# Optimization experiments

Hardware: AMD Instinct MI355X
Metric: run time of the kernel (lower is better)

The kernel has to match this reference:

```python
import jax, jax.numpy as jnp
import numpy as np
from jax import lax

B, T, F, H, O = 64, 2048, 128, 128, 128


def setup_inputs() -> dict:
    key = jax.random.key(0)
    ks = jax.random.split(key, 14)
    s = 1.0 / np.sqrt(H)  # torch default GRU/Linear init scale
    u = lambda k_, shp: jax.random.uniform(k_, shp, jnp.float32, -s, s)
    # sorted descending, as required by pack_padded_sequence(enforce_sorted=True)
    lengths = jnp.sort(jax.random.randint(ks[1], (B,), T // 2, T + 1))[::-1]
    return {
        'to_x': jax.random.normal(ks[0], (B, T, F), jnp.float32),
        'lengths': lengths,
        'enc_Wih': u(ks[2], (3 * H, F)), 'enc_Whh': u(ks[3], (3 * H, H)),
        'enc_bih': u(ks[4], (3 * H,)), 'enc_bhh': u(ks[5], (3 * H,)),
        'fc_W': u(ks[6], (H, H)), 'fc_b': u(ks[7], (H,)),
        'dec_Wih': u(ks[8], (3 * H, H)), 'dec_Whh': u(ks[9], (3 * H, H)),
        'dec_bih': u(ks[10], (3 * H,)), 'dec_bhh': u(ks[11], (3 * H,)),
        'out_W': u(ks[12], (O, H)), 'out_b': u(ks[13], (O,)),
    }


def _gru_gates(gi, gh, h):
    # PyTorch GRU cell: r,z gates then candidate n; gate order in weights is [r|z|n]
    ir, iz, inn = jnp.split(gi, 3, -1)
    hr, hz, hn = jnp.split(gh, 3, -1)
    r = jax.nn.sigmoid(ir + hr)
    z = jax.nn.sigmoid(iz + hz)
    n = jnp.tanh(inn + r * hn)
    return (1.0 - z) * n + z * h


def _forward(to_x, lengths, enc_Wih, enc_Whh, enc_bih, enc_bhh, fc_W, fc_b,
             dec_Wih, dec_Whh, dec_bih, dec_bhh, out_W, out_b):
    Bv, Tv, _ = to_x.shape
    Hv = enc_Whh.shape[1]
    # precompute all input projections for the encoder in one big GEMM
    gi_all = jnp.einsum('btf,gf->tbg', to_x, enc_Wih) + enc_bih  # [T,B,3H]
    valid = jnp.arange(Tv)[:, None] < lengths[None, :]  # [T,B]; packed-seq mask

    def enc_step(h, inp):
        gi_t, v_t = inp
        gh = h @ enc_Whh.T + enc_bhh
        h_new = _gru_gates(gi_t, gh, h)
        # packed GRU: hidden frozen once t >= length (final hidden per sequence)
        return jnp.where(v_t[:, None], h_new, h), None

    h_enc, _ = lax.scan(enc_step, jnp.zeros((Bv, Hv), to_x.dtype), (gi_all, valid))

    encoded = h_enc @ fc_W.T + fc_b  # encodeFc on last-layer final hidden

    def dec_cell(x, h):
        gi = x @ dec_Wih.T + dec_bih
        gh = h @ dec_Whh.T + dec_bhh
        return _gru_gates(gi, gh, h)

    # first decoder step: input = encoded, initial hidden = encoder final hidden
    y0 = dec_cell(encoded, h_enc)

    # previous output as both input and (implicitly) hidden state
    def dec_step(h, _):
        h_new = dec_cell(h, h)
        return h_new, h_new

    _, ys = lax.scan(dec_step, y0, None, length=Tv - 1)  # [T-1,B,H]
    dec_out = jnp.concatenate([y0[None], ys], axis=0)  # [T,B,H]
    return jnp.einsum('tbh,oh->bto', dec_out, out_W) + out_b  # [B,T,O]


def reference(to_x, lengths, enc_Wih, enc_Whh, enc_bih, enc_bhh, fc_W, fc_b,
              dec_Wih, dec_Whh, dec_bih, dec_bhh, out_W, out_b):
    return _forward(to_x, lengths, enc_Wih, enc_Whh, enc_bih, enc_bhh, fc_W, fc_b,
                    dec_Wih, dec_Whh, dec_bih, dec_bhh, out_W, out_b)
```

## Files before the change

### kernel.cpp

```cpp
#include <hip/hip_runtime.h>

namespace {

constexpr int kT = 2048;
constexpr int kH = 128;
constexpr int kB = 64;
constexpr int kG = 384;

__device__ __forceinline__ float fsigmoid(float x) {
    return 1.0f / (1.0f + __expf(-x));
}

__device__ __forceinline__ float ftanh(float x) {
    float xc = fminf(fmaxf(x, -15.0f), 15.0f);
    float e = __expf(2.0f * xc);
    return (e - 1.0f) / (e + 1.0f);
}

__device__ __forceinline__ void lds_barrier() {
    __builtin_amdgcn_sched_barrier(0);
    asm volatile("s_waitcnt lgkmcnt(0)" ::: "memory");
    __builtin_amdgcn_s_barrier();
    __builtin_amdgcn_sched_barrier(0);
}

__device__ __forceinline__ float qred(float x) {
    int y1 = __builtin_amdgcn_update_dpp(0, __float_as_int(x), 0xB1, 0xF, 0xF, true);
    x += __int_as_float(y1);
    int y2 = __builtin_amdgcn_update_dpp(0, __float_as_int(x), 0x4E, 0xF, 0xF, true);
    return x + __int_as_float(y2);
}

#define FMA4(acc, wrow, base)                      \
    acc = fmaf(v.x, wrow[(base) + 0], acc);        \
    acc = fmaf(v.y, wrow[(base) + 1], acc);        \
    acc = fmaf(v.z, wrow[(base) + 2], acc);        \
    acc = fmaf(v.w, wrow[(base) + 3], acc);

#define ST4(arr, base, vv)        \
    arr[(base) + 0] = (vv).x;     \
    arr[(base) + 1] = (vv).y;     \
    arr[(base) + 2] = (vv).z;     \
    arr[(base) + 3] = (vv).w;

#define ST4ADD(arr, base, va, vb)          \
    arr[(base) + 0] = (va).x + (vb).x;     \
    arr[(base) + 1] = (va).y + (vb).y;     \
    arr[(base) + 2] = (va).z + (vb).z;     \
    arr[(base) + 3] = (va).w + (vb).w;

__global__ __launch_bounds__(256, 2) void gi_gemm(
    const float* __restrict__ A, const float* __restrict__ W,
    const float* __restrict__ bias, float* __restrict__ G,
    int t0, int steps)
{
    __shared__ float As[128][68];
    __shared__ float Ws[128][68];
    const int m0 = blockIdx.x * 64;
    const int n0 = blockIdx.y * 64;
    const int b  = m0 / steps;
    const int tl = m0 % steps;
    const int tid = threadIdx.x;
    const float* Arow0 = A + ((size_t)b * kT + t0 + tl) * kH;

#pragma unroll
    for (int jj = 0; jj < 8; ++jj) {
        const int i = tid + jj * 256;
        const int r = i >> 5, cb = (i & 31) * 4;
        const float4 va = *reinterpret_cast<const float4*>(Arow0 + (size_t)r * kH + cb);
        As[cb + 0][r] = va.x; As[cb + 1][r] = va.y; As[cb + 2][r] = va.z; As[cb + 3][r] = va.w;
        const float4 vw = *reinterpret_cast<const float4*>(W + (size_t)(n0 + r) * kH + cb);
        Ws[cb + 0][r] = vw.x; Ws[cb + 1][r] = vw.y; Ws[cb + 2][r] = vw.z; Ws[cb + 3][r] = vw.w;
    }
    __syncthreads();

    const int tx = tid & 15, ty = tid >> 4;
    float acc[4][4] = {};
#pragma unroll 2
    for (int k = 0; k < 128; ++k) {
        const float4 a  = *reinterpret_cast<const float4*>(&As[k][ty * 4]);
        const float4 bv = *reinterpret_cast<const float4*>(&Ws[k][tx * 4]);
        const float av[4] = {a.x, a.y, a.z, a.w};
        const float bb[4] = {bv.x, bv.y, bv.z, bv.w};
#pragma unroll
        for (int r = 0; r < 4; ++r)
#pragma unroll
            for (int c = 0; c < 4; ++c) acc[r][c] = fmaf(av[r], bb[c], acc[r][c]);
    }
    const float4 b4 = *reinterpret_cast<const float4*>(bias + n0 + tx * 4);
    const float badd[4] = {b4.x, b4.y, b4.z, b4.w};
#pragma unroll
    for (int r = 0; r < 4; ++r) {
        float4 o;
        o.x = acc[r][0] + badd[0]; o.y = acc[r][1] + badd[1];
        o.z = acc[r][2] + badd[2]; o.w = acc[r][3] + badd[3];
        *reinterpret_cast<float4*>(G + (size_t)(m0 + ty * 4 + r) * kG + n0 + tx * 4) = o;
    }
}

__global__ __attribute__((amdgpu_flat_work_group_size(512, 512), amdgpu_waves_per_eu(2, 2)))
void enc_slab_kernel(
    const float* __restrict__ gslab, const int* __restrict__ lengths,
    const float* __restrict__ Whh, const float* __restrict__ bhh,
    float* __restrict__ hstate, float* __restrict__ out,
    int t0, int t1, int init, int final_slab)
{
    __shared__ __align__(16) float hb[2][kH];

    const int b = blockIdx.x;
    const int tid = threadIdx.x;
    const int j = tid >> 2;
    const int sub = tid & 3;
    const int kbase = sub * 32;
    const int len = lengths[b];

    float w[3][32];
#pragma unroll
    for (int cc = 0; cc < 8; ++cc) {
        const int kk = kbase + (((cc + 2 * sub) & 7) << 2);
        float4 v;
        v = *reinterpret_cast<const float4*>(Whh + (size_t)j * kH + kk);            ST4(w[0], cc * 4, v);
        v = *reinterpret_cast<const float4*>(Whh + (size_t)(kH + j) * kH + kk);     ST4(w[1], cc * 4, v);
        v = *reinterpret_cast<const float4*>(Whh + (size_t)(2 * kH + j) * kH + kk); ST4(w[2], cc * 4, v);
    }
    const float bh0 = bhh[j];
    const float bh1 = bhh[kH + j];
    const float bh2 = bhh[2 * kH + j];

    const float* gb = gslab + (size_t)b * (t1 - t0) * kG;
    float gr[4], gz[4], gn[4];
#define LOADG(s, tt)                                              \
    do {                                                          \
        const int tc = ((tt) < t1) ? (tt) : (t1 - 1);             \
        const float* gp = gb + (size_t)(tc - t0) * kG;            \
        gr[s] = gp[j]; gz[s] = gp[kH + j]; gn[s] = gp[2 * kH + j];\
    } while (0)
    LOADG(0, t0); LOADG(1, t0 + 1); LOADG(2, t0 + 2); LOADG(3, t0 + 3);

    if (tid < kH) hb[0][tid] = init ? 0.0f : hstate[(size_t)b * kH + tid];
    __syncthreads();

    int cur = 0;
    int tcap = (len + 3) & ~3;
    if (tcap > t1) tcap = t1;

#define ENC_STEP(s)                                                         \
    do {                                                                    \
        const int t = tb + (s);                                             \
        const float* hcur = hb[cur];                                        \
        float A0 = 0.f, A1 = 0.f, A2 = 0.f;                                 \
        _Pragma("unroll")                                                   \
        for (int cc = 0; cc < 8; ++cc) {                                    \
            const float4 v = *reinterpret_cast<const float4*>(              \
                hcur + kbase + (((cc + 2 * sub) & 7) << 2));                \
            FMA4(A0, w[0], cc * 4);                                         \
            FMA4(A1, w[1], cc * 4);                                         \
            FMA4(A2, w[2], cc * 4);                                         \
        }                                                                   \
        A0 = qred(A0); A1 = qred(A1); A2 = qred(A2);                        \
        const float hq = hcur[j];                                           \
        const float r = fsigmoid(gr[s] + A0 + bh0);                         \
        const float z = fsigmoid(gz[s] + A1 + bh1);                         \
        const float n = ftanh(gn[s] + r * (A2 + bh2));                      \
        const float hnew = (1.0f - z) * n + z * hq;                         \
        const float hc = (t < len) ? hnew : hq;                             \
        LOADG(s, t + 4);                                                    \
        const int nxt = cur ^ 1;                                            \
        if (sub == 0) hb[nxt][j] = hc;                                      \
        lds_barrier();                                                      \
        cur = nxt;                                                          \
    } while (0)

    for (int tb = t0; tb < tcap; tb += 4) {
        ENC_STEP(0); ENC_STEP(1); ENC_STEP(2); ENC_STEP(3);
    }
#undef ENC_STEP
#undef LOADG

    if (tid < kH) {
        hstate[(size_t)b * kH + tid] = hb[cur][tid];
        if (final_slab) out[((size_t)b * kT + 1) * kH + tid] = hb[cur][tid];
    }
}

__global__ __launch_bounds__(512, 2) void enc_fb_kernel(
    const float* __restrict__ to_x, const int* __restrict__ lengths,
    const float* __restrict__ Wih, const float* __restrict__ Whh,
    const float* __restrict__ bih, const float* __restrict__ bhh,
    float* __restrict__ out)
{
    __shared__ __align__(16) float hb2[2][132];
    __shared__ __align__(16) float xr[4][132];

    const int b = blockIdx.x;
    const int tid = threadIdx.x;
    const int j = tid >> 2;
    const int s4 = tid & 3;
    const int xh = s4 >> 1;
    const int sub = s4 & 1;
    const int len = lengths[b];
    const bool loader = (tid >= 480);
    const float* xrow = to_x + (size_t)b * kT * kH + (tid - 480) * 4;

    const float* W  = xh ? Whh : Wih;
    const float* bp = xh ? bhh : bih;

    float w[3][64];
#pragma unroll
    for (int r = 0; r < 3; ++r) {
        const float* rowp = W + (size_t)(r * kH + j) * kH + sub * 64;
#pragma unroll
        for (int k = 0; k < 64; k += 4) {
            const float4 v = *reinterpret_cast<const float4*>(rowp + k);
            ST4(w[r], k, v);
        }
    }
    const float bias0 = bp[j];
    const float bias1 = bp[kH + j];
    const float bias2 = bp[2 * kH + j];

    float4 xf0, xf1, xf2, xf3;
    if (tid < kH) hb2[0][tid] = 0.0f;
    if (loader) {
        xf0 = *reinterpret_cast<const float4*>(xrow + 0 * (size_t)kH);
        xf1 = *reinterpret_cast<const float4*>(xrow + 1 * (size_t)kH);
        xf2 = *reinterpret_cast<const float4*>(xrow + 2 * (size_t)kH);
        xf3 = *reinterpret_cast<const float4*>(xrow + 3 * (size_t)kH);
        *reinterpret_cast<float4*>(&xr[0][(tid - 480) * 4]) = xf0;
    }
    __syncthreads();

    int cur = 0;
    const int lenUp = (len + 3) & ~3;

#define FB_STEP(s, XFCUR, XFNEXT)                                          \
    do {                                                                   \
        const int t = t0 + (s);                                            \
        const float* src = (xh ? &hb2[cur][0] : &xr[s][0]) + sub * 64;     \
        float a0 = 0.f, a1 = 0.f, a2 = 0.f;                                \
        _Pragma("unroll")                                                  \
        for (int c = 0; c < 16; ++c) {                                     \
            const float4 v = *reinterpret_cast<const float4*>(src + c * 4);\
            FMA4(a0, w[0], c * 4);                                         \
            FMA4(a1, w[1], c * 4);                                         \
            FMA4(a2, w[2], c * 4);                                         \
        }                                                                  \
        a0 += __shfl_xor(a0, 1);                                           \
        a1 += __shfl_xor(a1, 1);                                           \
        a2 += __shfl_xor(a2, 1);                                           \
        a0 += bias0; a1 += bias1; a2 += bias2;                             \
        const float b0 = __shfl_xor(a0, 2);                                \
        const float b1 = __shfl_xor(a1, 2);                                \
        const float b2 = __shfl_xor(a2, 2);                                \
        const float hq  = hb2[cur][j];                                     \
        const float r   = fsigmoid(a0 + b0);                               \
        const float z   = fsigmoid(a1 + b1);                               \
        const float inn = xh ? b2 : a2;                                    \
        const float hn  = xh ? a2 : b2;                                    \
        const float n   = ftanh(inn + r * hn);                             \
        const float hnew = (1.0f - z) * n + z * hq;                        \
        const float hc = (t < len) ? hnew : hq;                            \
        if (loader) {                                                      \
            const int tc = ((t + 4) < len) ? (t + 4) : (len - 1);          \
            XFCUR = *reinterpret_cast<const float4*>(xrow + (size_t)tc * kH); \
        }                                                                  \
        const int nxt = cur ^ 1;                                           \
        if (s4 == 0) hb2[nxt][j] = hc;                                     \
        if (loader) *reinterpret_cast<float4*>(&xr[((s) + 1) & 3][(tid - 480) * 4]) = XFNEXT; \
        lds_barrier();                                                     \
        cur = nxt;                                                         \
    } while (0)

    for (int t0 = 0; t0 < lenUp; t0 += 4) {
        FB_STEP(0, xf0, xf1);
        FB_STEP(1, xf1, xf2);
        FB_STEP(2, xf2, xf3);
        FB_STEP(3, xf3, xf0);
    }
#undef FB_STEP

    if (tid < kH) out[((size_t)b * kT + 1) * kH + tid] = hb2[cur][tid];
}

__global__ void y0_kernel(
    const float* __restrict__ fcW, const float* __restrict__ fcb,
    const float* __restrict__ Wih, const float* __restrict__ Whh,
    const float* __restrict__ bih, const float* __restrict__ bhh,
    float* __restrict__ out)
{
    __shared__ float h[kH];
    __shared__ float enc[kH];
    __shared__ float gbuf[768];

    const int b = blockIdx.x;
    const int tid = threadIdx.x;

    if (tid < kH) h[tid] = out[((size_t)b * kT + 1) * kH + tid];
    __syncthreads();

    if (tid < kH) {
        float s = fcb[tid];
        const float* row = fcW + (size_t)tid * kH;
#pragma unroll 4
        for (int k = 0; k < kH; k += 4) {
            const float4 v = *reinterpret_cast<const float4*>(row + k);
            s = fmaf(v.x, h[k + 0], s);
            s = fmaf(v.y, h[k + 1], s);
            s = fmaf(v.z, h[k + 2], s);
            s = fmaf(v.w, h[k + 3], s);
        }
        enc[tid] = s;
    }
    __syncthreads();

    for (int rr = 0; rr < 3; ++rr) {
        const int row = tid + 256 * rr;
        const float* Wr;
        const float* src;
        float s;
        if (row < 384) { Wr = Wih + (size_t)row * kH;         src = enc; s = bih[row]; }
        else           { Wr = Whh + (size_t)(row - 384) * kH; src = h;   s = bhh[row - 384]; }
#pragma unroll 4
        for (int k = 0; k < kH; k += 4) {
            const float4 v = *reinterpret_cast<const float4*>(Wr + k);
            s = fmaf(v.x, src[k + 0], s);
            s = fmaf(v.y, src[k + 1], s);
            s = fmaf(v.z, src[k + 2], s);
            s = fmaf(v.w, src[k + 3], s);
        }
        gbuf[row] = s;
    }
    __syncthreads();

    if (tid < kH) {
        const float r = fsigmoid(gbuf[tid] + gbuf[384 + tid]);
        const float z = fsigmoid(gbuf[128 + tid] + gbuf[512 + tid]);
        const float n = ftanh(gbuf[256 + tid] + r * gbuf[640 + tid]);
        out[(size_t)b * kT * kH + tid] = (1.0f - z) * n + z * h[tid];
    }
}

__global__ __attribute__((amdgpu_flat_work_group_size(512, 512), amdgpu_waves_per_eu(2, 2)))
void dec_kernel(
    const float* __restrict__ Wih, const float* __restrict__ Whh,
    const float* __restrict__ bih, const float* __restrict__ bhh,
    float* __restrict__ out)
{
    __shared__ __align__(16) float hb[2][kH];
    __shared__ int lastbad;

    const int b     = blockIdx.x;
    const int tid   = threadIdx.x;
    const int q     = tid >> 2;
    const int sub   = tid & 3;
    const int kbase = sub * 32;
    constexpr float kTol = 2e-6f;

    float w[4][32];
#pragma unroll
    for (int cc = 0; cc < 8; ++cc) {
        const int kk = kbase + (((cc + 2 * sub) & 7) << 2);
        float4 vi, vh;
        vi = *reinterpret_cast<const float4*>(Wih + (size_t)q * kH + kk);
        vh = *reinterpret_cast<const float4*>(Whh + (size_t)q * kH + kk);
        ST4ADD(w[0], cc * 4, vi, vh);
        vi = *reinterpret_cast<const float4*>(Wih + (size_t)(kH + q) * kH + kk);
        vh = *reinterpret_cast<const float4*>(Whh + (size_t)(kH + q) * kH + kk);
        ST4ADD(w[1], cc * 4, vi, vh);
        vi = *reinterpret_cast<const float4*>(Wih + (size_t)(2 * kH + q) * kH + kk);
        ST4(w[2], cc * 4, vi);
        vh = *reinterpret_cast<const float4*>(Whh + (size_t)(2 * kH + q) * kH + kk);
        ST4(w[3], cc * 4, vh);
    }
    const float brz0 = bih[q] + bhh[q];
    const float brz1 = bih[kH + q] + bhh[kH + q];
    const float bin  = bih[2 * kH + q];
    const float bhn  = bhh[2 * kH + q];

    if (tid < kH) hb[0][tid] = out[(size_t)b * kT * kH + tid];
    if (tid == 0) lastbad = 0;
    __syncthreads();

    float* orow = out + (size_t)b * kT * kH + q;

    int cur = 0;
    int tfill = kT;
    for (int t = 1; t < kT; ++t) {
        const float* hcur = hb[cur];
        float a0 = 0.f, a1 = 0.f, a2 = 0.f, a3 = 0.f;
#pragma unroll
        for (int cc = 0; cc < 8; ++cc) {
            const float4 v = *reinterpret_cast<const float4*>(
                hcur + kbase + (((cc + 2 * sub) & 7) << 2));
            FMA4(a0, w[0], cc * 4);
            FMA4(a1, w[1], cc * 4);
            FMA4(a2, w[2], cc * 4);
            FMA4(a3, w[3], cc * 4);
        }
        a0 = qred(a0); a1 = qred(a1); a2 = qred(a2); a3 = qred(a3);

        const float hq = hcur[q];
        const float r = fsigmoid(a0 + brz0);
        const float z = fsigmoid(a1 + brz1);
        const float n = ftanh(a2 + bin + r * (a3 + bhn));
        const float hnew = (1.0f - z) * n + z * hq;

        const int nxt = cur ^ 1;
        if (sub == 0) {
            hb[nxt][q] = hnew;
            orow[(size_t)t * kH] = hnew;
            if (fabsf(hnew - hq) > kTol) lastbad = t;
        }
        lds_barrier();
        cur = nxt;
        if (lastbad != t) { tfill = t + 1; break; }
    }

    if (tfill < kT) {
        const int c = tid & 31;
        const float4 hv = *reinterpret_cast<const float4*>(&hb[cur][c * 4]);
        for (int tt = tfill + (tid >> 5); tt < kT; tt += 16) {
            *reinterpret_cast<float4*>(out + ((size_t)b * kT + tt) * kH + c * 4) = hv;
        }
    }
}

__global__ __launch_bounds__(256, 1) void proj_kernel(
    const float* __restrict__ Wo, const float* __restrict__ ob,
    float* __restrict__ out)
{
    __shared__ float As[128][68];
    __shared__ float Ws[128][132];
    const int m0 = blockIdx.x * 64;
    const int tid = threadIdx.x;

#pragma unroll
    for (int jj = 0; jj < 8; ++jj) {
        const int i = tid + jj * 256;
        const int r = i >> 5, cb = (i & 31) * 4;
        const float4 v = *reinterpret_cast<const float4*>(out + (size_t)(m0 + r) * kH + cb);
        As[cb + 0][r] = v.x; As[cb + 1][r] = v.y; As[cb + 2][r] = v.z; As[cb + 3][r] = v.w;
    }
#pragma unroll
    for (int jj = 0; jj < 16; ++jj) {
        const int i = tid + jj * 256;
        const int o = i >> 5, cb = (i & 31) * 4;
        const float4 v = *reinterpret_cast<const float4*>(Wo + (size_t)o * kH + cb);
        Ws[cb + 0][o] = v.x; Ws[cb + 1][o] = v.y; Ws[cb + 2][o] = v.z; Ws[cb + 3][o] = v.w;
    }
    __syncthreads();

    const int tx = tid & 15, ty = tid >> 4;
    float acc[4][8] = {};
#pragma unroll 2
    for (int k = 0; k < 128; ++k) {
        const float4 a  = *reinterpret_cast<const float4*>(&As[k][ty * 4]);
        const float4 b0 = *reinterpret_cast<const float4*>(&Ws[k][tx * 4]);
        const float4 b1 = *reinterpret_cast<const float4*>(&Ws[k][64 + tx * 4]);
        const float av[4] = {a.x, a.y, a.z, a.w};
        const float bb[8] = {b0.x, b0.y, b0.z, b0.w, b1.x, b1.y, b1.z, b1.w};
#pragma unroll
        for (int r = 0; r < 4; ++r)
#pragma unroll
            for (int c = 0; c < 8; ++c) acc[r][c] = fmaf(av[r], bb[c], acc[r][c]);
    }
    const float4 o0 = *reinterpret_cast<const float4*>(ob + tx * 4);
    const float4 o1 = *reinterpret_cast<const float4*>(ob + 64 + tx * 4);
    const float ba[8] = {o0.x, o0.y, o0.z, o0.w, o1.x, o1.y, o1.z, o1.w};
#pragma unroll
    for (int r = 0; r < 4; ++r) {
        float4 s0, s1;
        s0.x = acc[r][0] + ba[0]; s0.y = acc[r][1] + ba[1];
        s0.z = acc[r][2] + ba[2]; s0.w = acc[r][3] + ba[3];
        s1.x = acc[r][4] + ba[4]; s1.y = acc[r][5] + ba[5];
        s1.z = acc[r][6] + ba[6]; s1.w = acc[r][7] + ba[7];
        float* rowp = out + (size_t)(m0 + ty * 4 + r) * kH;
        *reinterpret_cast<float4*>(rowp + tx * 4)      = s0;
        *reinterpret_cast<float4*>(rowp + 64 + tx * 4) = s1;
    }
}

}

extern "C" void kernel_launch(void* const* d_in, const int* in_sizes, int n_in,
                              void* d_out, int out_size, void* d_ws, size_t ws_size,
                              hipStream_t stream) {
    (void)in_sizes; (void)n_in; (void)out_size;

    const float* to_x    = (const float*)d_in[0];
    const int*   lengths = (const int*)d_in[1];
    const float* eWih    = (const float*)d_in[2];
    const float* eWhh    = (const float*)d_in[3];
    const float* ebih    = (const float*)d_in[4];
    const float* ebhh    = (const float*)d_in[5];
    const float* fcW     = (const float*)d_in[6];
    const float* fcb     = (const float*)d_in[7];
    const float* dWih    = (const float*)d_in[8];
    const float* dWhh    = (const float*)d_in[9];
    const float* dbih    = (const float*)d_in[10];
    const float* dbhh    = (const float*)d_in[11];
    const float* oW      = (const float*)d_in[12];
    const float* obv     = (const float*)d_in[13];
    float* out = (float*)d_out;

    const size_t hstate_bytes = (size_t)kB * kH * sizeof(float);
    auto gi_bytes = [](int steps) { return (size_t)kB * steps * kG * sizeof(float); };

    int steps = 0;
    if      (ws_size >= hstate_bytes + gi_bytes(2048)) steps = 2048;
    else if (ws_size >= hstate_bytes + gi_bytes(512))  steps = 512;
    else if (ws_size >= hstate_bytes + gi_bytes(128))  steps = 128;

    if (steps) {
        float* hstate = (float*)d_ws;
        float* gi = (float*)((char*)d_ws + hstate_bytes);
        const int nslab = kT / steps;
        for (int i = 0; i < nslab; ++i) {
            const int t0 = i * steps;
            gi_gemm<<<dim3(steps, 6), 256, 0, stream>>>(to_x, eWih, ebih, gi, t0, steps);
            enc_slab_kernel<<<kB, 512, 0, stream>>>(gi, lengths, eWhh, ebhh, hstate, out,
                                                    t0, t0 + steps, i == 0, i == nslab - 1);
        }
    } else {
        enc_fb_kernel<<<kB, 512, 0, stream>>>(to_x, lengths, eWih, eWhh, ebih, ebhh, out);
    }
    y0_kernel<<<kB, 256, 0, stream>>>(fcW, fcb, dWih, dWhh, dbih, dbhh, out);
    dec_kernel<<<kB, 512, 0, stream>>>(dWih, dWhh, dbih, dbhh, out);
    proj_kernel<<<2048, 256, 0, stream>>>(oW, obv, out);
}
```

Baseline: 1.784 ms.

## Process two batch sequences per encoder block sharing register-resident weights

```diff
diff --git a/kernel.cpp b/kernel.cpp
--- a/kernel.cpp
+++ b/kernel.cpp
@@ -36,6 +36,12 @@
     acc = fmaf(v.y, wrow[(base) + 1], acc);        \
     acc = fmaf(v.z, wrow[(base) + 2], acc);        \
     acc = fmaf(v.w, wrow[(base) + 3], acc);
+
+#define FMA4V(acc, wrow, base, vv)                   \
+    acc = fmaf((vv).x, wrow[(base) + 0], acc);       \
+    acc = fmaf((vv).y, wrow[(base) + 1], acc);       \
+    acc = fmaf((vv).z, wrow[(base) + 2], acc);       \
+    acc = fmaf((vv).w, wrow[(base) + 3], acc);
 
 #define ST4(arr, base, vv)        \
     arr[(base) + 0] = (vv).x;     \
@@ -56,8 +62,8 @@
 {
     __shared__ float As[128][68];
     __shared__ float Ws[128][68];
-    const int m0 = blockIdx.x * 64;
-    const int n0 = blockIdx.y * 64;
+    const int m0 = blockIdx.y * 64;
+    const int n0 = blockIdx.x * 64;
     const int b  = m0 / steps;
     const int tl = m0 % steps;
     const int tid = threadIdx.x;
@@ -99,20 +105,23 @@
 }
 
 __global__ __attribute__((amdgpu_flat_work_group_size(512, 512), amdgpu_waves_per_eu(2, 2)))
-void enc_slab_kernel(
+void enc_pair_kernel(
     const float* __restrict__ gslab, const int* __restrict__ lengths,
     const float* __restrict__ Whh, const float* __restrict__ bhh,
     float* __restrict__ hstate, float* __restrict__ out,
     int t0, int t1, int init, int final_slab)
 {
-    __shared__ __align__(16) float hb[2][kH];
-
-    const int b = blockIdx.x;
+    __shared__ __align__(16) float hb[2][2][kH];
+
+    const int bp = blockIdx.x;
+    const int b0 = 2 * bp, b1 = 2 * bp + 1;
     const int tid = threadIdx.x;
     const int j = tid >> 2;
     const int sub = tid & 3;
     const int kbase = sub * 32;
-    const int len = lengths[b];
+    const int len0 = lengths[b0];
+    const int len1 = lengths[b1];
+    const int steps = t1 - t0;
 
     float w[3][32];
 #pragma unroll
@@ -127,48 +136,67 @@
     const float bh1 = bhh[kH + j];
     const float bh2 = bhh[2 * kH + j];
 
-    const float* gb = gslab + (size_t)b * (t1 - t0) * kG;
-    float gr[4], gz[4], gn[4];
-#define LOADG(s, tt)                                              \
-    do {                                                          \
-        const int tc = ((tt) < t1) ? (tt) : (t1 - 1);             \
-        const float* gp = gb + (size_t)(tc - t0) * kG;            \
-        gr[s] = gp[j]; gz[s] = gp[kH + j]; gn[s] = gp[2 * kH + j];\
+    const float* gb0 = gslab + (size_t)b0 * steps * kG;
+    const float* gb1 = gslab + (size_t)b1 * steps * kG;
+    float g0r[4], g0z[4], g0n[4], g1r[4], g1z[4], g1n[4];
+#define LOADG(s, tt)                                                          \
+    do {                                                                      \
+        const int tc0 = ((tt) < len0) ? (tt) : (len0 - 1);                    \
+        const int tc1 = ((tt) < len1) ? (tt) : (len1 - 1);                    \
+        const float* gp0 = gb0 + (size_t)(tc0 - t0) * kG;                     \
+        const float* gp1 = gb1 + (size_t)(tc1 - t0) * kG;                     \
+        g0r[s] = gp0[j]; g0z[s] = gp0[kH + j]; g0n[s] = gp0[2 * kH + j];      \
+        g1r[s] = gp1[j]; g1z[s] = gp1[kH + j]; g1n[s] = gp1[2 * kH + j];      \
     } while (0)
     LOADG(0, t0); LOADG(1, t0 + 1); LOADG(2, t0 + 2); LOADG(3, t0 + 3);
 
-    if (tid < kH) hb[0][tid] = init ? 0.0f : hstate[(size_t)b * kH + tid];
+    if (tid < kH)                    hb[0][0][tid]       = init ? 0.0f : hstate[(size_t)b0 * kH + tid];
+    else if (tid < 2 * kH)           hb[0][1][tid - kH]  = init ? 0.0f : hstate[(size_t)b1 * kH + tid - kH];
     __syncthreads();
 
     int cur = 0;
-    int tcap = (len + 3) & ~3;
+    const int lenMax = (len0 > len1) ? len0 : len1;
+    int tcap = (lenMax + 3) & ~3;
     if (tcap > t1) tcap = t1;
 
-#define ENC_STEP(s)                                                         \
-    do {                                                                    \
-        const int t = tb + (s);                                             \
-        const float* hcur = hb[cur];                                        \
-        float A0 = 0.f, A1 = 0.f, A2 = 0.f;                                 \
-        _Pragma("unroll")                                                   \
-        for (int cc = 0; cc < 8; ++cc) {                                    \
-            const float4 v = *reinterpret_cast<const float4*>(              \
-                hcur + kbase + (((cc + 2 * sub) & 7) << 2));                \
-            FMA4(A0, w[0], cc * 4);                                         \
-            FMA4(A1, w[1], cc * 4);                                         \
-            FMA4(A2, w[2], cc * 4);                                         \
-        }                                                                   \
-        A0 = qred(A0); A1 = qred(A1); A2 = qred(A2);                        \
-        const float hq = hcur[j];                                           \
-        const float r = fsigmoid(gr[s] + A0 + bh0);                         \
-        const float z = fsigmoid(gz[s] + A1 + bh1);                         \
-        const float n = ftanh(gn[s] + r * (A2 + bh2));                      \
-        const float hnew = (1.0f - z) * n + z * hq;                         \
-        const float hc = (t < len) ? hnew : hq;                             \
-        LOADG(s, t + 4);                                                    \
-        const int nxt = cur ^ 1;                                            \
-        if (sub == 0) hb[nxt][j] = hc;                                      \
-        lds_barrier();                                                      \
-        cur = nxt;                                                          \
+#define ENC_STEP(s)                                                          \
+    do {                                                                     \
+        const int t = tb + (s);                                              \
+        const float* h0c = hb[cur][0];                                       \
+        const float* h1c = hb[cur][1];                                       \
+        float A0 = 0.f, A1 = 0.f, A2 = 0.f;                                  \
+        float B0 = 0.f, B1 = 0.f, B2 = 0.f;                                  \
+        _Pragma("unroll")                                                    \
+        for (int cc = 0; cc < 8; ++cc) {                                     \
+            const int off = kbase + (((cc + 2 * sub) & 7) << 2);             \
+            const float4 v0 = *reinterpret_cast<const float4*>(h0c + off);   \
+            const float4 v1 = *reinterpret_cast<const float4*>(h1c + off);   \
+            FMA4V(A0, w[0], cc * 4, v0);                                     \
+            FMA4V(A1, w[1], cc * 4, v0);                                     \
+            FMA4V(A2, w[2], cc * 4, v0);                                     \
+            FMA4V(B0, w[0], cc * 4, v1);                                     \
+            FMA4V(B1, w[1], cc * 4, v1);                                     \
+            FMA4V(B2, w[2], cc * 4, v1);                                     \
+        }                                                                    \
+        A0 = qred(A0); A1 = qred(A1); A2 = qred(A2);                         \
+        B0 = qred(B0); B1 = qred(B1); B2 = qred(B2);                         \
+        const float hq0 = h0c[j];                                            \
+        const float hq1 = h1c[j];                                            \
+        const float r0 = fsigmoid(g0r[s] + A0 + bh0);                        \
+        const float z0 = fsigmoid(g0z[s] + A1 + bh1);                        \
+        const float n0 = ftanh(g0n[s] + r0 * (A2 + bh2));                    \
+        const float r1 = fsigmoid(g1r[s] + B0 + bh0);                        \
+        const float z1 = fsigmoid(g1z[s] + B1 + bh1);                        \
+        const float n1 = ftanh(g1n[s] + r1 * (B2 + bh2));                    \
+        const float hn0 = (1.0f - z0) * n0 + z0 * hq0;                       \
+        const float hn1 = (1.0f - z1) * n1 + z1 * hq1;                       \
+        const float hc0 = (t < len0) ? hn0 : hq0;                            \
+        const float hc1 = (t < len1) ? hn1 : hq1;                            \
+        LOADG(s, t + 4);                                                     \
+        const int nxt = cur ^ 1;                                             \
+        if (sub == 0) { hb[nxt][0][j] = hc0; hb[nxt][1][j] = hc1; }          \
+        lds_barrier();                                                       \
+        cur = nxt;                                                           \
     } while (0)
 
     for (int tb = t0; tb < tcap; tb += 4) {
@@ -178,8 +206,11 @@
 #undef LOADG
 
     if (tid < kH) {
-        hstate[(size_t)b * kH + tid] = hb[cur][tid];
-        if (final_slab) out[((size_t)b * kT + 1) * kH + tid] = hb[cur][tid];
+        hstate[(size_t)b0 * kH + tid] = hb[cur][0][tid];
+        if (final_slab) out[((size_t)b0 * kT + 1) * kH + tid] = hb[cur][0][tid];
+    } else if (tid < 2 * kH) {
+        hstate[(size_t)b1 * kH + (tid - kH)] = hb[cur][1][tid - kH];
+        if (final_slab) out[((size_t)b1 * kT + 1) * kH + (tid - kH)] = hb[cur][1][tid - kH];
     }
 }
 
@@ -517,9 +548,9 @@
         const int nslab = kT / steps;
         for (int i = 0; i < nslab; ++i) {
             const int t0 = i * steps;
-            gi_gemm<<<dim3(steps, 6), 256, 0, stream>>>(to_x, eWih, ebih, gi, t0, steps);
-            enc_slab_kernel<<<kB, 512, 0, stream>>>(gi, lengths, eWhh, ebhh, hstate, out,
-                                                    t0, t0 + steps, i == 0, i == nslab - 1);
+            gi_gemm<<<dim3(6, steps), 256, 0, stream>>>(to_x, eWih, ebih, gi, t0, steps);
+            enc_pair_kernel<<<kB / 2, 512, 0, stream>>>(gi, lengths, eWhh, ebhh, hstate, out,
+                                                        t0, t0 + steps, i == 0, i == nslab - 1);
         }
     } else {
         enc_fb_kernel<<<kB, 512, 0, stream>>>(to_x, lengths, eWih, eWhh, ebih, ebhh, out);
```

After: 2.859 ms. 1.6x slower.
